# Optimization experiments

Measured on AMD Instinct MI355X. Metric: run time of the kernel, lower is better.

Reference implementation:

```python
import jax, jax.numpy as jnp
import numpy as np

N = 100000      # nodes
E = 1600000     # edges (before self-loops)
F_IN = 128      # num_feats
H = 128         # dim_hidden
C = 64          # num_classes
EPS = 1e-5      # BatchNorm eps
SLOPE = 0.2     # LeakyReLU negative slope (PyG GATConv default)


def setup_inputs() -> dict:
    key = jax.random.key(0)
    ks = jax.random.split(key, 8)
    x = jax.random.normal(ks[0], (N, F_IN), jnp.float32)
    edge_index = jax.random.randint(ks[1], (2, E), 0, N, dtype=jnp.int32)
    W0 = jax.random.normal(ks[2], (F_IN, H), jnp.float32) * (1.0 / np.sqrt(F_IN))
    a_src0 = jax.random.normal(ks[3], (H,), jnp.float32) * 0.1
    a_dst0 = jax.random.normal(ks[4], (H,), jnp.float32) * 0.1
    W1 = jax.random.normal(ks[5], (H, C), jnp.float32) * (1.0 / np.sqrt(H))
    a_src1 = jax.random.normal(ks[6], (C,), jnp.float32) * 0.1
    a_dst1 = jax.random.normal(ks[7], (C,), jnp.float32) * 0.1
    return {
        "x": x, "edge_index": edge_index,
        "W0": W0, "a_src0": a_src0, "a_dst0": a_dst0,
        "g0": jnp.ones((H,), jnp.float32), "b0": jnp.zeros((H,), jnp.float32),
        "W1": W1, "a_src1": a_src1, "a_dst1": a_dst1,
        "g1": jnp.ones((C,), jnp.float32), "b1": jnp.zeros((C,), jnp.float32),
    }


def _gat_conv(x, src, dst, W, a_s, a_d):
    # x: [N, d_in]; src/dst: [E'] (self-loops included). heads=1, bias=False.
    h = x @ W                                   # [N, d_out]
    s = h @ a_s                                 # [N] alpha_src per node
    d = h @ a_d                                 # [N] alpha_dst per node
    logits = jax.nn.leaky_relu(s[src] + d[dst], SLOPE)   # [E']
    # segment softmax over incoming edges of each dst node
    m = jax.ops.segment_max(logits, dst, num_segments=N)
    w = jnp.exp(logits - m[dst])
    denom = jax.ops.segment_sum(w, dst, num_segments=N)
    coef = w / denom[dst]                       # [E']
    return jax.ops.segment_sum(coef[:, None] * h[src], dst, num_segments=N)


def _batch_norm(x, g, b):
    mu = jnp.mean(x, axis=0)
    var = jnp.var(x, axis=0)
    return (x - mu) * jax.lax.rsqrt(var + EPS) * g + b


def reference(x, edge_index, W0, a_src0, a_dst0, g0, b0, W1, a_src1, a_dst1, g1, b1):
    loops = jnp.arange(N, dtype=edge_index.dtype)
    src = jnp.concatenate([edge_index[0], loops])
    dst = jnp.concatenate([edge_index[1], loops])
    h = _gat_conv(x, src, dst, W0, a_src0, a_dst0)
    h = jax.nn.relu(_batch_norm(h, g0, b0))
    h = _gat_conv(h, src, dst, W1, a_src1, a_dst1)
    return jax.nn.relu(_batch_norm(h, g1, b1))
```

## Files before the change

kernel.cpp:

```cpp
#include <hip/hip_runtime.h>
#include <hip/hip_bf16.h>
#include <cmath>

#define BN_EPS 1e-5f
#define SLOPE 0.2f

typedef __attribute__((ext_vector_type(8))) short bf16x8;
typedef __attribute__((ext_vector_type(4))) float f32x4;

__device__ __forceinline__ float lrelu(float x) { return x >= 0.f ? x : SLOPE * x; }
__device__ __forceinline__ float bfl(unsigned u) { return __uint_as_float(u << 16); }
__device__ __forceinline__ float bfh(unsigned u) { return __uint_as_float(u & 0xffff0000u); }
__device__ __forceinline__ float bf2f(unsigned short u) { return __uint_as_float((unsigned)u << 16); }
__device__ __forceinline__ unsigned short f2bf(float f) {
    __hip_bfloat16 h = __float2bfloat16(f);
    return *reinterpret_cast<unsigned short*>(&h);
}

__global__ __launch_bounds__(512) void k_hist(const int* __restrict__ ei, int E, int n,
                                              int nbk, int* __restrict__ gcnt) {
    __shared__ int h[512];
    int t = threadIdx.x;
    for (int i = t; i < nbk; i += 512) h[i] = 0;
    __syncthreads();
    int base = blockIdx.x * 8192;
    int tot = E + n;
#pragma unroll
    for (int k = 0; k < 16; ++k) {
        int i = base + k * 512 + t;
        if (i < tot) {
            int dst = (i < E) ? ei[E + i] : (i - E);
            atomicAdd(&h[dst >> 8], 1);
        }
    }
    __syncthreads();
    for (int i = t; i < nbk; i += 512)
        if (h[i]) atomicAdd(&gcnt[i], h[i]);
}

__global__ __launch_bounds__(512) void k_bscan(const int* __restrict__ gcnt,
                                               int* __restrict__ gbase,
                                               int* __restrict__ gnext, int nbk) {
    __shared__ int tmp[512];
    int t = threadIdx.x;
    int v = (t < nbk) ? gcnt[t] : 0;
    tmp[t] = v;
    __syncthreads();
    for (int off = 1; off < 512; off <<= 1) {
        int a = (t >= off) ? tmp[t - off] : 0;
        __syncthreads();
        tmp[t] += a;
        __syncthreads();
    }
    int ex = tmp[t] - v;
    if (t < nbk) { gbase[t] = ex; gnext[t] = ex; }
    if (t == nbk - 1) gbase[nbk] = tmp[t];
}

__global__ __launch_bounds__(512) void k_bucket(const int* __restrict__ ei, int E, int n,
                                                int nbk, int* __restrict__ gnext,
                                                int2* __restrict__ bbuf) {
    __shared__ int h[512], off[512], c2[512];
    int t = threadIdx.x;
    for (int i = t; i < nbk; i += 512) { h[i] = 0; c2[i] = 0; }
    __syncthreads();
    int base = blockIdx.x * 8192;
    int tot = E + n;
    int srcv[16], dstv[16];
#pragma unroll
    for (int k = 0; k < 16; ++k) {
        int i = base + k * 512 + t;
        dstv[k] = -1;
        if (i < tot) {
            int s, d;
            if (i < E) { s = ei[i]; d = ei[E + i]; }
            else       { s = i - E; d = s; }
            srcv[k] = s; dstv[k] = d;
            atomicAdd(&h[d >> 8], 1);
        }
    }
    __syncthreads();
    for (int i = t; i < nbk; i += 512)
        if (h[i]) off[i] = atomicAdd(&gnext[i], h[i]);
    __syncthreads();
#pragma unroll
    for (int k = 0; k < 16; ++k) {
        int d = dstv[k];
        if (d >= 0) {
            int b = d >> 8;
            int r = atomicAdd(&c2[b], 1);
            bbuf[off[b] + r] = make_int2(srcv[k], d);
        }
    }
}

__global__ __launch_bounds__(256) void k_csr2(const int2* __restrict__ bbuf,
                                              const int* __restrict__ gbase,
                                              int* __restrict__ rowp, int* __restrict__ csr,
                                              int n, int nbk) {
    __shared__ int cnt[256], scn[256];
    int b = blockIdx.x;
    int t = threadIdx.x;
    int beg = gbase[b], end = gbase[b + 1];
    int node0 = b << 8;
    cnt[t] = 0;
    __syncthreads();
    for (int i = beg + t; i < end; i += 256)
        atomicAdd(&cnt[bbuf[i].y & 255], 1);
    __syncthreads();
    int v = cnt[t];
    scn[t] = v;
    __syncthreads();
    for (int off = 1; off < 256; off <<= 1) {
        int a = (t >= off) ? scn[t - off] : 0;
        __syncthreads();
        scn[t] += a;
        __syncthreads();
    }
    int ex = scn[t] - v;
    if (node0 + t < n) rowp[node0 + t] = beg + ex;
    if (b == nbk - 1 && t == 0) rowp[n] = end;
    cnt[t] = ex;
    __syncthreads();
    for (int i = beg + t; i < end; i += 256) {
        int2 e = bbuf[i];
        int pos = atomicAdd(&cnt[e.y & 255], 1);
        csr[beg + pos] = e.x;
    }
}

template <int CD>
__global__ void k_packw(const float* __restrict__ W, unsigned short* __restrict__ Wp) {
    int idx = blockIdx.x * 256 + threadIdx.x;
    if (idx >= 128 * CD) return;
    int k = idx / CD, nG = idx % CD;
    int nt = nG >> 4, nn = nG & 15, ks = k >> 5, g = (k >> 3) & 3, j = k & 7;
    Wp[(((nt * 4 + ks) * 64) + g * 16 + nn) * 8 + j] = f2bf(W[idx]);
}

template <int CD, bool BN_IN, bool XBF>
__global__ __launch_bounds__(256) void k_gemm_mfma(
    const void* __restrict__ Xv, const unsigned short* __restrict__ Wp,
    const float* __restrict__ bnsums, const float* __restrict__ gg,
    const float* __restrict__ bb, const float* __restrict__ a_s,
    const float* __restrict__ a_d, unsigned short* __restrict__ hb,
    float* __restrict__ s_out, float* __restrict__ d_out, int n) {
    constexpr int NT = CD / 16;
    const float* Xf = (const float*)Xv;
    const unsigned short* Xh = (const unsigned short*)Xv;
    __shared__ unsigned short wl[128 * CD];
    __shared__ float sc[128], sh[128];
    int t = threadIdx.x;
    for (int i = t * 8; i < 128 * CD; i += 2048)
        *(uint4*)&wl[i] = *(const uint4*)&Wp[i];
    if constexpr (BN_IN) {
        if (t < 128) {
            float invn = 1.f / (float)n;
            float mu = bnsums[t] * invn;
            float var = bnsums[128 + t] * invn - mu * mu;
            float s = gg[t] * rsqrtf(var + BN_EPS);
            sc[t] = s;
            sh[t] = bb[t] - mu * s;
        }
    }
    __syncthreads();
    int w = t >> 6, l = t & 63;
    int m = l & 15, g = l >> 4;
    int r0 = blockIdx.x * 64;
    int row = r0 + w * 16 + m;
    bool rv = row < n;
    bf16x8 af[4];
#pragma unroll
    for (int ks = 0; ks < 4; ++ks) {
        int c0 = ks * 32 + g * 8;
        float xv[8];
        if constexpr (XBF) {
            uint4 u = make_uint4(0, 0, 0, 0);
            if (rv) u = *(const uint4*)&Xh[(size_t)row * 128 + c0];
            unsigned uu[4] = {u.x, u.y, u.z, u.w};
#pragma unroll
            for (int q = 0; q < 4; ++q) { xv[2 * q] = bfl(uu[q]); xv[2 * q + 1] = bfh(uu[q]); }
        } else {
            float4 x0 = make_float4(0.f, 0.f, 0.f, 0.f), x1 = x0;
            if (rv) {
                x0 = *(const float4*)&Xf[(size_t)row * 128 + c0];
                x1 = *(const float4*)&Xf[(size_t)row * 128 + c0 + 4];
            }
            xv[0] = x0.x; xv[1] = x0.y; xv[2] = x0.z; xv[3] = x0.w;
            xv[4] = x1.x; xv[5] = x1.y; xv[6] = x1.z; xv[7] = x1.w;
        }
        bf16x8 a;
#pragma unroll
        for (int j = 0; j < 8; ++j) {
            float v = xv[j];
            if constexpr (BN_IN) v = fmaxf(0.f, v * sc[c0 + j] + sh[c0 + j]);
            a[j] = (short)f2bf(v);
        }
        af[ks] = a;
    }
    f32x4 acc[NT];
#pragma unroll
    for (int i = 0; i < NT; ++i) acc[i] = (f32x4){0.f, 0.f, 0.f, 0.f};
#pragma unroll
    for (int ks = 0; ks < 4; ++ks) {
#pragma unroll
        for (int nt = 0; nt < NT; ++nt) {
            bf16x8 bfr = *(bf16x8*)&wl[(((nt * 4 + ks) * 64) + l) * 8];
            acc[nt] = __builtin_amdgcn_mfma_f32_16x16x32_bf16(af[ks], bfr, acc[nt], 0, 0, 0);
        }
    }
    float ps[4] = {0.f, 0.f, 0.f, 0.f}, pd[4] = {0.f, 0.f, 0.f, 0.f};
#pragma unroll
    for (int nt = 0; nt < NT; ++nt) {
        float as = a_s[nt * 16 + m], ad = a_d[nt * 16 + m];
#pragma unroll
        for (int r = 0; r < 4; ++r) {
            ps[r] += acc[nt][r] * as;
            pd[r] += acc[nt][r] * ad;
        }
    }
#pragma unroll
    for (int off = 1; off < 16; off <<= 1) {
#pragma unroll
        for (int r = 0; r < 4; ++r) {
            ps[r] += __shfl_xor(ps[r], off);
            pd[r] += __shfl_xor(pd[r], off);
        }
    }
    __syncthreads();
    unsigned short* ot = wl;
#pragma unroll
    for (int nt = 0; nt < NT; ++nt) {
#pragma unroll
        for (int r = 0; r < 4; ++r)
            ot[(w * 16 + g * 4 + r) * CD + nt * 16 + m] = f2bf(acc[nt][r]);
    }
    if (m == 0) {
        int orow = r0 + w * 16 + g * 4;
#pragma unroll
        for (int r = 0; r < 4; ++r) {
            if (orow + r < n) { s_out[orow + r] = ps[r]; d_out[orow + r] = pd[r]; }
        }
    }
    __syncthreads();
    constexpr int CPR = CD / 8;
    for (int c = t; c < 64 * CPR; c += 256) {
        int rr = c / CPR, cc = c % CPR;
        if (r0 + rr < n)
            *(uint4*)&hb[(size_t)(r0 + rr) * CD + cc * 8] = *(uint4*)&ot[rr * CD + cc * 8];
    }
}

template <int DIM, bool OUT_BF>
__global__ __launch_bounds__(256) void k_agg(
    const unsigned short* __restrict__ hb, const float* __restrict__ s,
    const float* __restrict__ d, const int* __restrict__ rowp,
    const int* __restrict__ csr, void* __restrict__ outv, int n) {
    constexpr int LPE = DIM / 8;
    constexpr int EPW = 64 / LPE;
    int wid = (blockIdx.x * blockDim.x + threadIdx.x) >> 6;
    int lane = threadIdx.x & 63;
    if (wid >= n) return;
    int beg = rowp[wid], end = rowp[wid + 1];
    float dv = d[wid];
    int grp = lane / LPE, ll = lane % LPE;
    float acc[8] = {};
    float denom = 0.f;
    for (int e = beg + grp; e < end; e += EPW * 2) {
        int eB = e + EPW;
        bool vB = eB < end;
        int iA = csr[e];
        int iB = vB ? csr[eB] : iA;
        float wA = __expf(lrelu(s[iA] + dv));
        float wB = vB ? __expf(lrelu(s[iB] + dv)) : 0.f;
        uint4 pA = *(const uint4*)&hb[(size_t)iA * DIM + ll * 8];
        uint4 pB = *(const uint4*)&hb[(size_t)iB * DIM + ll * 8];
        denom += wA + wB;
        unsigned ua[4] = {pA.x, pA.y, pA.z, pA.w};
        unsigned ub[4] = {pB.x, pB.y, pB.z, pB.w};
#pragma unroll
        for (int q = 0; q < 4; ++q) {
            acc[2 * q]     += wA * bfl(ua[q]) + wB * bfl(ub[q]);
            acc[2 * q + 1] += wA * bfh(ua[q]) + wB * bfh(ub[q]);
        }
    }
#pragma unroll
    for (int off = LPE; off < 64; off <<= 1) {
        denom += __shfl_xor(denom, off);
#pragma unroll
        for (int f = 0; f < 8; ++f) acc[f] += __shfl_xor(acc[f], off);
    }
    if (grp == 0) {
        float inv = 1.f / denom;
        if constexpr (OUT_BF) {
            unsigned u[4];
#pragma unroll
            for (int q = 0; q < 4; ++q)
                u[q] = (unsigned)f2bf(acc[2 * q] * inv) |
                       ((unsigned)f2bf(acc[2 * q + 1] * inv) << 16);
            *(uint4*)((unsigned short*)outv + (size_t)wid * DIM + ll * 8) =
                make_uint4(u[0], u[1], u[2], u[3]);
        } else {
            float* orow = (float*)outv + (size_t)wid * DIM + ll * 8;
            *(float4*)&orow[0] = make_float4(acc[0] * inv, acc[1] * inv, acc[2] * inv, acc[3] * inv);
            *(float4*)&orow[4] = make_float4(acc[4] * inv, acc[5] * inv, acc[6] * inv, acc[7] * inv);
        }
    }
}

template <int CD, bool XBF>
__global__ void k_bn_stats(const void* __restrict__ xv, float* __restrict__ sums, int n) {
    const float* xf = (const float*)xv;
    const unsigned short* xh = (const unsigned short*)xv;
    constexpr int RPB = 256 / CD;
    int t = threadIdx.x;
    int c = t & (CD - 1);
    int rl = t / CD;
    float s = 0.f, sq = 0.f;
    for (int r = blockIdx.x * RPB + rl; r < n; r += gridDim.x * RPB) {
        float v = XBF ? bf2f(xh[(size_t)r * CD + c]) : xf[(size_t)r * CD + c];
        s += v;
        sq += v * v;
    }
    __shared__ float ls[256], lq[256];
    ls[t] = s; lq[t] = sq;
    __syncthreads();
    if (t < CD) {
#pragma unroll
        for (int j = 1; j < RPB; ++j) { s += ls[t + j * CD]; sq += lq[t + j * CD]; }
        atomicAdd(&sums[c], s);
        atomicAdd(&sums[CD + c], sq);
    }
}

template <int CD>
__global__ void k_bn_apply(const float* __restrict__ x, const float* __restrict__ sums,
                           const float* __restrict__ g, const float* __restrict__ b,
                           float* __restrict__ out, int n) {
    size_t i = (size_t)blockIdx.x * blockDim.x + threadIdx.x;
    size_t tot = (size_t)n * CD;
    if (i >= tot) return;
    int c = (int)(i & (CD - 1));
    float invn = 1.f / (float)n;
    float mu = sums[c] * invn;
    float var = sums[CD + c] * invn - mu * mu;
    float v = (x[i] - mu) * rsqrtf(var + BN_EPS) * g[c] + b[c];
    out[i] = fmaxf(v, 0.f);
}

extern "C" void kernel_launch(void* const* d_in, const int* in_sizes, int n_in,
                              void* d_out, int out_size, void* d_ws, size_t ws_size,
                              hipStream_t stream) {
    const float* x   = (const float*)d_in[0];
    const int*   ei  = (const int*)  d_in[1];
    const float* W0  = (const float*)d_in[2];
    const float* as0 = (const float*)d_in[3];
    const float* ad0 = (const float*)d_in[4];
    const float* g0  = (const float*)d_in[5];
    const float* b0  = (const float*)d_in[6];
    const float* W1  = (const float*)d_in[7];
    const float* as1 = (const float*)d_in[8];
    const float* ad1 = (const float*)d_in[9];
    const float* g1  = (const float*)d_in[10];
    const float* b1  = (const float*)d_in[11];
    float* out = (float*)d_out;

    const int N_ = in_sizes[0] / 128;
    const int E_ = in_sizes[1] / 2;
    const int TOT = E_ + N_;
    const int nbk = (N_ + 255) >> 8;

    char* p = (char*)d_ws;
    unsigned short* hb   = (unsigned short*)p; p += (size_t)N_ * 128 * 2;
    unsigned short* aggB = (unsigned short*)p; p += (size_t)N_ * 128 * 2;
    float* agg1 = (float*)p;                   p += (size_t)N_ * 64 * 4;
    int2* bbuf  = (int2*)p;                    p += (size_t)TOT * 8;
    float* s0   = (float*)p;                   p += (size_t)N_ * 4;
    float* d0   = (float*)p;                   p += (size_t)N_ * 4;
    float* bns0 = (float*)p;                   p += 256 * 4;
    float* bns1 = (float*)p;                   p += 128 * 4;
    int* gcnt   = (int*)p;                     p += 512 * 4;
    int* gbase  = (int*)p;                     p += 514 * 4;
    int* gnext  = (int*)p;                     p += 512 * 4;
    int* rowp   = (int*)p;                     p += (size_t)(N_ + 2) * 4;
    int* csr    = (int*)p;                     p += (size_t)TOT * 4;
    unsigned short* Wp0 = (unsigned short*)p;  p += 128 * 128 * 2;
    unsigned short* Wp1 = (unsigned short*)p;  p += 128 * 64 * 2;

    hipMemsetAsync(gcnt, 0, 512 * 4, stream);
    hipMemsetAsync(bns0, 0, 384 * 4, stream);

    const int ebBlocks = (TOT + 8191) / 8192;
    k_hist<<<ebBlocks, 512, 0, stream>>>(ei, E_, N_, nbk, gcnt);
    k_bscan<<<1, 512, 0, stream>>>(gcnt, gbase, gnext, nbk);
    k_bucket<<<ebBlocks, 512, 0, stream>>>(ei, E_, N_, nbk, gnext, bbuf);
    k_csr2<<<nbk, 256, 0, stream>>>(bbuf, gbase, rowp, csr, N_, nbk);

    k_packw<128><<<64, 256, 0, stream>>>(W0, Wp0);
    k_packw<64><<<32, 256, 0, stream>>>(W1, Wp1);

    const int gemmBlocks = (N_ + 63) / 64;
    const int waveBlocks = (N_ + 3) / 4;

    k_gemm_mfma<128, false, false><<<gemmBlocks, 256, 0, stream>>>(
        x, Wp0, nullptr, nullptr, nullptr, as0, ad0, hb, s0, d0, N_);
    k_agg<128, true><<<waveBlocks, 256, 0, stream>>>(hb, s0, d0, rowp, csr, aggB, N_);
    k_bn_stats<128, true><<<256, 256, 0, stream>>>(aggB, bns0, N_);

    k_gemm_mfma<64, true, true><<<gemmBlocks, 256, 0, stream>>>(
        aggB, Wp1, bns0, g0, b0, as1, ad1, hb, s0, d0, N_);
    k_agg<64, false><<<waveBlocks, 256, 0, stream>>>(hb, s0, d0, rowp, csr, agg1, N_);
    k_bn_stats<64, false><<<256, 256, 0, stream>>>(agg1, bns1, N_);
    k_bn_apply<64><<<(int)(((size_t)N_ * 64 + 255) / 256), 256, 0, stream>>>(
        agg1, bns1, g1, b1, out, N_);
}
```

Baseline: 398.7 us.

## Assign one sub-wave group per node in aggregation, reuse bucket ranks, merge weight packing

The aggregation kernels now give each destination node LPE lanes (16 for the 128-wide layer, 8 for the 64-wide one) instead of a full 64-lane wave. Each group walks the node's edge list sequentially, which removes the cross-lane shuffle reduction and the idle lanes on low-degree nodes, and the grid sizes shrink to match. The risk is load imbalance and less memory-level parallelism on high-degree nodes. The bucket kernel reuses the rank returned by the first shared-memory atomic, dropping the second atomic pass, and the two weight-packing launches are merged into one.

Result: no change. 402.4 us (+0.9%).

```diff
diff --git a/kernel.cpp b/kernel.cpp
--- a/kernel.cpp
+++ b/kernel.cpp
@@ -60,13 +60,13 @@
 __global__ __launch_bounds__(512) void k_bucket(const int* __restrict__ ei, int E, int n,
                                                 int nbk, int* __restrict__ gnext,
                                                 int2* __restrict__ bbuf) {
-    __shared__ int h[512], off[512], c2[512];
-    int t = threadIdx.x;
-    for (int i = t; i < nbk; i += 512) { h[i] = 0; c2[i] = 0; }
+    __shared__ int h[512], off[512];
+    int t = threadIdx.x;
+    for (int i = t; i < nbk; i += 512) h[i] = 0;
     __syncthreads();
     int base = blockIdx.x * 8192;
     int tot = E + n;
-    int srcv[16], dstv[16];
+    int srcv[16], dstv[16], rnk[16];
 #pragma unroll
     for (int k = 0; k < 16; ++k) {
         int i = base + k * 512 + t;
@@ -76,7 +76,7 @@
             if (i < E) { s = ei[i]; d = ei[E + i]; }
             else       { s = i - E; d = s; }
             srcv[k] = s; dstv[k] = d;
-            atomicAdd(&h[d >> 8], 1);
+            rnk[k] = atomicAdd(&h[d >> 8], 1);
         }
     }
     __syncthreads();
@@ -86,11 +86,8 @@
 #pragma unroll
     for (int k = 0; k < 16; ++k) {
         int d = dstv[k];
-        if (d >= 0) {
-            int b = d >> 8;
-            int r = atomicAdd(&c2[b], 1);
-            bbuf[off[b] + r] = make_int2(srcv[k], d);
-        }
+        if (d >= 0)
+            bbuf[off[d >> 8] + rnk[k]] = make_int2(srcv[k], d);
     }
 }
 
@@ -129,13 +126,21 @@
     }
 }
 
-template <int CD>
-__global__ void k_packw(const float* __restrict__ W, unsigned short* __restrict__ Wp) {
+__global__ void k_packw2(const float* __restrict__ W0, const float* __restrict__ W1,
+                         unsigned short* __restrict__ Wp0, unsigned short* __restrict__ Wp1) {
     int idx = blockIdx.x * 256 + threadIdx.x;
-    if (idx >= 128 * CD) return;
-    int k = idx / CD, nG = idx % CD;
-    int nt = nG >> 4, nn = nG & 15, ks = k >> 5, g = (k >> 3) & 3, j = k & 7;
-    Wp[(((nt * 4 + ks) * 64) + g * 16 + nn) * 8 + j] = f2bf(W[idx]);
+    if (idx < 128 * 128) {
+        int k = idx >> 7, nG = idx & 127;
+        int nt = nG >> 4, nn = nG & 15, ks = k >> 5, g = (k >> 3) & 3, j = k & 7;
+        Wp0[(((nt * 4 + ks) * 64) + g * 16 + nn) * 8 + j] = f2bf(W0[idx]);
+    } else {
+        int i2 = idx - 128 * 128;
+        if (i2 < 128 * 64) {
+            int k = i2 >> 6, nG = i2 & 63;
+            int nt = nG >> 4, nn = nG & 15, ks = k >> 5, g = (k >> 3) & 3, j = k & 7;
+            Wp1[(((nt * 4 + ks) * 64) + g * 16 + nn) * 8 + j] = f2bf(W1[i2]);
+        }
+    }
 }
 
 template <int CD, bool BN_IN, bool XBF>
@@ -257,22 +262,21 @@
     const float* __restrict__ d, const int* __restrict__ rowp,
     const int* __restrict__ csr, void* __restrict__ outv, int n) {
     constexpr int LPE = DIM / 8;
-    constexpr int EPW = 64 / LPE;
-    int wid = (blockIdx.x * blockDim.x + threadIdx.x) >> 6;
-    int lane = threadIdx.x & 63;
+    int gid = blockIdx.x * blockDim.x + threadIdx.x;
+    int wid = gid / LPE;
+    int ll = gid & (LPE - 1);
     if (wid >= n) return;
     int beg = rowp[wid], end = rowp[wid + 1];
     float dv = d[wid];
-    int grp = lane / LPE, ll = lane % LPE;
     float acc[8] = {};
     float denom = 0.f;
-    for (int e = beg + grp; e < end; e += EPW * 2) {
-        int eB = e + EPW;
-        bool vB = eB < end;
+    for (int e = beg; e < end; e += 2) {
+        int e1 = e + 1;
+        bool v1 = e1 < end;
         int iA = csr[e];
-        int iB = vB ? csr[eB] : iA;
+        int iB = v1 ? csr[e1] : iA;
         float wA = __expf(lrelu(s[iA] + dv));
-        float wB = vB ? __expf(lrelu(s[iB] + dv)) : 0.f;
+        float wB = v1 ? __expf(lrelu(s[iB] + dv)) : 0.f;
         uint4 pA = *(const uint4*)&hb[(size_t)iA * DIM + ll * 8];
         uint4 pB = *(const uint4*)&hb[(size_t)iB * DIM + ll * 8];
         denom += wA + wB;
@@ -284,27 +288,19 @@
             acc[2 * q + 1] += wA * bfh(ua[q]) + wB * bfh(ub[q]);
         }
     }
-#pragma unroll
-    for (int off = LPE; off < 64; off <<= 1) {
-        denom += __shfl_xor(denom, off);
-#pragma unroll
-        for (int f = 0; f < 8; ++f) acc[f] += __shfl_xor(acc[f], off);
-    }
-    if (grp == 0) {
-        float inv = 1.f / denom;
-        if constexpr (OUT_BF) {
-            unsigned u[4];
-#pragma unroll
-            for (int q = 0; q < 4; ++q)
-                u[q] = (unsigned)f2bf(acc[2 * q] * inv) |
-                       ((unsigned)f2bf(acc[2 * q + 1] * inv) << 16);
-            *(uint4*)((unsigned short*)outv + (size_t)wid * DIM + ll * 8) =
-                make_uint4(u[0], u[1], u[2], u[3]);
-        } else {
-            float* orow = (float*)outv + (size_t)wid * DIM + ll * 8;
-            *(float4*)&orow[0] = make_float4(acc[0] * inv, acc[1] * inv, acc[2] * inv, acc[3] * inv);
-            *(float4*)&orow[4] = make_float4(acc[4] * inv, acc[5] * inv, acc[6] * inv, acc[7] * inv);
-        }
+    float inv = 1.f / denom;
+    if constexpr (OUT_BF) {
+        unsigned u[4];
+#pragma unroll
+        for (int q = 0; q < 4; ++q)
+            u[q] = (unsigned)f2bf(acc[2 * q] * inv) |
+                   ((unsigned)f2bf(acc[2 * q + 1] * inv) << 16);
+        *(uint4*)((unsigned short*)outv + (size_t)wid * DIM + ll * 8) =
+            make_uint4(u[0], u[1], u[2], u[3]);
+    } else {
+        float* orow = (float*)outv + (size_t)wid * DIM + ll * 8;
+        *(float4*)&orow[0] = make_float4(acc[0] * inv, acc[1] * inv, acc[2] * inv, acc[3] * inv);
+        *(float4*)&orow[4] = make_float4(acc[4] * inv, acc[5] * inv, acc[6] * inv, acc[7] * inv);
     }
 }
 
@@ -396,20 +392,20 @@
     k_bucket<<<ebBlocks, 512, 0, stream>>>(ei, E_, N_, nbk, gnext, bbuf);
     k_csr2<<<nbk, 256, 0, stream>>>(bbuf, gbase, rowp, csr, N_, nbk);
 
-    k_packw<128><<<64, 256, 0, stream>>>(W0, Wp0);
-    k_packw<64><<<32, 256, 0, stream>>>(W1, Wp1);
+    k_packw2<<<96, 256, 0, stream>>>(W0, W1, Wp0, Wp1);
 
     const int gemmBlocks = (N_ + 63) / 64;
-    const int waveBlocks = (N_ + 3) / 4;
+    const int aggBlocks128 = (N_ + 15) / 16;
+    const int aggBlocks64  = (N_ + 31) / 32;
 
     k_gemm_mfma<128, false, false><<<gemmBlocks, 256, 0, stream>>>(
         x, Wp0, nullptr, nullptr, nullptr, as0, ad0, hb, s0, d0, N_);
-    k_agg<128, true><<<waveBlocks, 256, 0, stream>>>(hb, s0, d0, rowp, csr, aggB, N_);
+    k_agg<128, true><<<aggBlocks128, 256, 0, stream>>>(hb, s0, d0, rowp, csr, aggB, N_);
     k_bn_stats<128, true><<<256, 256, 0, stream>>>(aggB, bns0, N_);
 
     k_gemm_mfma<64, true, true><<<gemmBlocks, 256, 0, stream>>>(
         aggB, Wp1, bns0, g0, b0, as1, ad1, hb, s0, d0, N_);
-    k_agg<64, false><<<waveBlocks, 256, 0, stream>>>(hb, s0, d0, rowp, csr, agg1, N_);
+    k_agg<64, false><<<aggBlocks64, 256, 0, stream>>>(hb, s0, d0, rowp, csr, agg1, N_);
     k_bn_stats<64, false><<<256, 256, 0, stream>>>(agg1, bns1, N_);
     k_bn_apply<64><<<(int)(((size_t)N_ * 64 + 255) / 256), 256, 0, stream>>>(
         agg1, bns1, g1, b1, out, N_);
```
